# Performance work log

Measured on AMD Instinct MI355X. Metric: run time of the kernel, lower is better.

The kernel has to match this reference:

```python
import jax, jax.numpy as jnp
import numpy as np

N, E, C_IN, C_OUT = 50000, 800000, 64, 64
BN_EPS = 1e-5


def _batchnorm(h, gamma, beta):
    # Training-mode BatchNorm1d: batch statistics over dim 0, biased variance.
    mean = h.mean(axis=0)
    var = h.var(axis=0)  # ddof=0, matches PyTorch normalization stats
    return gamma * (h - mean) * jax.lax.rsqrt(var + BN_EPS) + beta


def setup_inputs() -> dict:
    key = jax.random.key(0)
    ks = jax.random.split(key, 6)
    x = jax.random.normal(ks[0], (N, C_IN), dtype=jnp.float32)
    edge_index = jax.random.randint(ks[1], (2, E), 0, N, dtype=jnp.int32)
    edge_weight = jax.random.uniform(ks[2], (E,), dtype=jnp.float32)
    s1 = 1.0 / np.sqrt(C_IN).astype(np.float32)
    s2 = 1.0 / np.sqrt(2 * C_IN).astype(np.float32)
    pool_W = jax.random.uniform(ks[3], (C_IN, C_IN), jnp.float32, -s1, s1)
    pool_b = jnp.zeros((C_IN,), jnp.float32)
    final_W = jax.random.uniform(ks[4], (2 * C_IN, C_OUT), jnp.float32, -s2, s2)
    final_b = jnp.zeros((C_OUT,), jnp.float32)
    return {
        "x": x,
        "edge_index": edge_index,
        "edge_weight": edge_weight,
        "pool_W": pool_W,
        "pool_b": pool_b,
        "bn_pool_gamma": jnp.ones((C_IN,), jnp.float32),
        "bn_pool_beta": jnp.zeros((C_IN,), jnp.float32),
        "final_W": final_W,
        "final_b": final_b,
        "bn_final_gamma": jnp.ones((C_OUT,), jnp.float32),
        "bn_final_beta": jnp.zeros((C_OUT,), jnp.float32),
        "coef": jnp.float32(0.5),
    }


def reference(x, edge_index, edge_weight, pool_W, pool_b, bn_pool_gamma,
              bn_pool_beta, final_W, final_b, bn_final_gamma, bn_final_beta,
              coef):
    src, dst = edge_index[0], edge_index[1]
    # gather src node features, scale by edge weight  -> [E, C_IN]
    edge_feat = x[src] * (1.0 + coef * edge_weight[:, None])
    pooled = edge_feat @ pool_W + pool_b              # [E, C_IN]
    pooled = jax.nn.relu(_batchnorm(pooled, bn_pool_gamma, bn_pool_beta))
    # scatter-max into destination nodes; empty segments -> 0 (pooled >= 0)
    agg = jax.ops.segment_max(pooled, dst, num_segments=x.shape[0])
    agg = jnp.maximum(agg, 0.0)                       # fill -inf (empty) with 0
    h = jnp.concatenate([x, agg], axis=-1) @ final_W + final_b  # [N, C_OUT]
    h = _batchnorm(h, bn_final_gamma, bn_final_beta)
    return jax.nn.relu(h)
```

## Files before the change

### kernel.cpp

```cpp
#include <hip/hip_runtime.h>
#include <hip/hip_fp16.h>
#include <math.h>
#include <float.h>

#define BN_EPS 1e-5f
#define SLOTS 64


typedef __attribute__((ext_vector_type(8))) short bf16x8;
typedef __attribute__((ext_vector_type(4))) float f32x4;

__device__ inline unsigned short f2bf(float f) {
    unsigned u = __float_as_uint(f);
    return (unsigned short)((u + 0x7fffu + ((u >> 16) & 1u)) >> 16);
}
__device__ inline float bf2f(unsigned short h) {
    return __uint_as_float(((unsigned)h) << 16);
}

__global__ __launch_bounds__(256) void k_scatter(const int* __restrict__ src,
                          const int* __restrict__ dst,
                          const float* __restrict__ w, const float* __restrict__ coef_p,
                          int* __restrict__ cnt, unsigned* __restrict__ csr, int E) {
    int i = blockIdx.x * blockDim.x + threadIdx.x;
    if (i >= E) return;
    const float coef = *coef_p;
    int sn = src[i], tn = dst[i];
    float s = fmaf(coef, w[i], 1.0f);
    unsigned hs = (unsigned)__half_as_ushort(__float2half(s));
    int pos = atomicAdd(&cnt[tn], 1);
    if (pos < SLOTS) csr[(size_t)tn * SLOTS + pos] = ((unsigned)sn << 16) | hs;
}

__global__ __launch_bounds__(256, 4) void k_gemm_pool(const float* __restrict__ x,
                            const float* __restrict__ W,
                            unsigned short* __restrict__ ybf, int nrows) {
    __shared__ unsigned short Wt[64 * 72];
    for (int i = threadIdx.x; i < 64 * 64; i += 256) {
        int k = i >> 6, n = i & 63;
        Wt[n * 72 + k] = f2bf(W[i]);
    }
    __syncthreads();
    const int lane = threadIdx.x & 63;
    const int wave = threadIdx.x >> 6;
    const int quad = lane >> 4;
    const int ln = lane & 15;
    bf16x8 Bf[2][4];
#pragma unroll
    for (int kc = 0; kc < 2; ++kc)
#pragma unroll
        for (int ct = 0; ct < 4; ++ct)
            Bf[kc][ct] = *(const bf16x8*)&Wt[(ct * 16 + ln) * 72 + kc * 32 + quad * 8];
    const int T = (nrows + 15) >> 4;
    const int gw = blockIdx.x * 4 + wave;
    const int nw = gridDim.x * 4;
    for (int t = gw; t < T; t += nw) {
        const int row = t * 16 + ln;
        bf16x8 af[2];
        if (row < nrows) {
            const float* xr = x + (size_t)row * 64;
#pragma unroll
            for (int kc = 0; kc < 2; ++kc) {
                float4 p = *(const float4*)(xr + kc * 32 + quad * 8);
                float4 q = *(const float4*)(xr + kc * 32 + quad * 8 + 4);
                bf16x8 a;
                a[0] = (short)f2bf(p.x); a[1] = (short)f2bf(p.y);
                a[2] = (short)f2bf(p.z); a[3] = (short)f2bf(p.w);
                a[4] = (short)f2bf(q.x); a[5] = (short)f2bf(q.y);
                a[6] = (short)f2bf(q.z); a[7] = (short)f2bf(q.w);
                af[kc] = a;
            }
        } else {
            bf16x8 z;
#pragma unroll
            for (int j = 0; j < 8; ++j) z[j] = 0;
            af[0] = z; af[1] = z;
        }
        f32x4 acc[4];
#pragma unroll
        for (int ct = 0; ct < 4; ++ct) { acc[ct][0]=0.f; acc[ct][1]=0.f; acc[ct][2]=0.f; acc[ct][3]=0.f; }
#pragma unroll
        for (int ct = 0; ct < 4; ++ct) {
            acc[ct] = __builtin_amdgcn_mfma_f32_16x16x32_bf16(af[0], Bf[0][ct], acc[ct], 0, 0, 0);
            acc[ct] = __builtin_amdgcn_mfma_f32_16x16x32_bf16(af[1], Bf[1][ct], acc[ct], 0, 0, 0);
        }
#pragma unroll
        for (int r = 0; r < 4; ++r) {
            int ro = t * 16 + quad * 4 + r;
            if (ro < nrows) {
#pragma unroll
                for (int ct = 0; ct < 4; ++ct)
                    ybf[(size_t)ro * 64 + ct * 16 + ln] = f2bf(acc[ct][r]);
            }
        }
    }
}

__global__ __launch_bounds__(256) void k_gather_max(const unsigned short* __restrict__ ybf,
                             const unsigned* __restrict__ csr, const int* __restrict__ cnt,
                             float* __restrict__ M, float* __restrict__ partials, int nrows) {
    int t = blockIdx.x * blockDim.x + threadIdx.x;
    int node = t >> 4;
    int sub = threadIdx.x & 15;
    int rg = threadIdx.x >> 4;
    int c0 = sub * 4;
    size_t base = (size_t)node * SLOTS;
    int dg = 0;
    if (node < nrows) { dg = cnt[node]; if (dg > SLOTS) dg = SLOTS; }
    float m0 = -FLT_MAX, m1 = -FLT_MAX, m2 = -FLT_MAX, m3 = -FLT_MAX;
    float s1[4] = {0, 0, 0, 0}, s2[4] = {0, 0, 0, 0};
    for (int k0 = 0; k0 < dg; k0 += 16) {
        int kk = k0 + sub;
        unsigned pk = (kk < dg) ? csr[base + kk] : 0u;
        int cnt16 = dg - k0; if (cnt16 > 16) cnt16 = 16;
        for (int j = 0; j < cnt16; ++j) {
            unsigned r = (unsigned)__shfl((int)pk, j, 16);
            int sn = r >> 16;
            float sv = __half2float(__ushort_as_half((unsigned short)(r & 0xffffu)));
            ushort4 uv = *(const ushort4*)&ybf[(size_t)sn * 64 + c0];
            float v0 = sv * bf2f(uv.x), v1 = sv * bf2f(uv.y);
            float v2 = sv * bf2f(uv.z), v3 = sv * bf2f(uv.w);
            m0 = fmaxf(m0, v0); s1[0] += v0; s2[0] = fmaf(v0, v0, s2[0]);
            m1 = fmaxf(m1, v1); s1[1] += v1; s2[1] = fmaf(v1, v1, s2[1]);
            m2 = fmaxf(m2, v2); s1[2] += v2; s2[2] = fmaf(v2, v2, s2[2]);
            m3 = fmaxf(m3, v3); s1[3] += v3; s2[3] = fmaf(v3, v3, s2[3]);
        }
    }
    if (node < nrows)
        *(float4*)&M[(size_t)node * 64 + c0] = make_float4(m0, m1, m2, m3);
    __shared__ float red[16][68];
#pragma unroll
    for (int j = 0; j < 4; ++j) red[rg][c0 + j] = s1[j];
    __syncthreads();
    if (rg == 0) {
#pragma unroll
        for (int j = 0; j < 4; ++j) {
            float tt = 0.0f;
            for (int r = 0; r < 16; ++r) tt += red[r][c0 + j];
            partials[(size_t)blockIdx.x * 128 + c0 + j] = tt;
        }
    }
    __syncthreads();
#pragma unroll
    for (int j = 0; j < 4; ++j) red[rg][c0 + j] = s2[j];
    __syncthreads();
    if (rg == 0) {
#pragma unroll
        for (int j = 0; j < 4; ++j) {
            float tt = 0.0f;
            for (int r = 0; r < 16; ++r) tt += red[r][c0 + j];
            partials[(size_t)blockIdx.x * 128 + 64 + c0 + j] = tt;
        }
    }
}

__global__ __launch_bounds__(256) void k_red1(const float* __restrict__ partials, int P,
                                              float* __restrict__ p2) {
    int c = threadIdx.x & 127;
    int half = threadIdx.x >> 7;
    float acc = 0.0f;
    for (int r = blockIdx.x * 2 + half; r < P; r += 256)
        acc += partials[(size_t)r * 128 + c];
    __shared__ float sh[256];
    sh[threadIdx.x] = acc;
    __syncthreads();
    if (half == 0) p2[(size_t)blockIdx.x * 128 + c] = sh[c] + sh[128 + c];
}

__global__ __launch_bounds__(1024) void k_red2(const float* __restrict__ p2,
                             const float* __restrict__ pool_b, const float* __restrict__ gamma,
                             const float* __restrict__ beta, float invE,
                             float* __restrict__ coef) {
    int c = threadIdx.x & 127;
    int seg = threadIdx.x >> 7;
    float acc = 0.0f;
    for (int r = seg; r < 128; r += 8) acc += p2[(size_t)r * 128 + c];
    __shared__ float red[8][128];
    red[seg][c] = acc;
    __syncthreads();
    if (seg == 0) {
        float tt = 0.0f;
#pragma unroll
        for (int s = 0; s < 8; ++s) tt += red[s][c];
        red[0][c] = tt;
    }
    __syncthreads();
    if (threadIdx.x < 64) {
        int c0 = threadIdx.x;
        float S1 = red[0][c0], S2 = red[0][64 + c0];
        float s1 = S1 * invE;
        float b = pool_b[c0];
        float mean = s1 + b;
        float ex2 = S2 * invE + 2.0f * b * s1 + b * b;
        float var = ex2 - mean * mean;
        float a = gamma[c0] * rsqrtf(var + BN_EPS);
        coef[c0] = a;
        coef[64 + c0] = beta[c0] - a * s1;
    }
}

__global__ __launch_bounds__(1024) void k_red2f(const float* __restrict__ p2,
                             const float* __restrict__ gamma, const float* __restrict__ beta,
                             float invN, float* __restrict__ coef) {
    int c = threadIdx.x & 127;
    int seg = threadIdx.x >> 7;
    float acc = 0.0f;
    for (int r = seg; r < 128; r += 8) acc += p2[(size_t)r * 128 + c];
    __shared__ float red[8][128];
    red[seg][c] = acc;
    __syncthreads();
    if (seg == 0) {
        float tt = 0.0f;
#pragma unroll
        for (int s = 0; s < 8; ++s) tt += red[s][c];
        red[0][c] = tt;
    }
    __syncthreads();
    if (threadIdx.x < 64) {
        int c0 = threadIdx.x;
        float mean = red[0][c0] * invN;
        float var = red[0][64 + c0] * invN - mean * mean;
        float a = gamma[c0] * rsqrtf(var + BN_EPS);
        coef[c0] = a;
        coef[64 + c0] = beta[c0] - a * mean;
    }
}

__global__ __launch_bounds__(256, 2) void k_final_gemm(const float* __restrict__ x,
                             const float* __restrict__ M, const float* __restrict__ coef,
                             const float* __restrict__ W, const float* __restrict__ b,
                             float* __restrict__ h, float* __restrict__ partials, int nrows) {
    __shared__ unsigned short Wt[64 * 136];
    __shared__ float hp[128];
    for (int i = threadIdx.x; i < 128 * 64; i += 256) {
        int k = i >> 6, n = i & 63;
        Wt[n * 136 + k] = f2bf(W[i]);
    }
    if (threadIdx.x < 128) hp[threadIdx.x] = 0.0f;
    __syncthreads();
    const int lane = threadIdx.x & 63;
    const int wave = threadIdx.x >> 6;
    const int quad = lane >> 4;
    const int ln = lane & 15;
    bf16x8 Bf[4][4];
#pragma unroll
    for (int kc = 0; kc < 4; ++kc)
#pragma unroll
        for (int ct = 0; ct < 4; ++ct)
            Bf[kc][ct] = *(const bf16x8*)&Wt[(ct * 16 + ln) * 136 + kc * 32 + quad * 8];
    float bias[4];
#pragma unroll
    for (int ct = 0; ct < 4; ++ct) bias[ct] = b[ct * 16 + ln];
    float ca[2][8], cd[2][8];
#pragma unroll
    for (int g = 0; g < 2; ++g) {
        int ch = g * 32 + quad * 8;
#pragma unroll
        for (int j = 0; j < 8; ++j) {
            ca[g][j] = coef[ch + j];
            cd[g][j] = coef[64 + ch + j];
        }
    }
    float ls1[4] = {0, 0, 0, 0}, ls2[4] = {0, 0, 0, 0};
    const int T = (nrows + 15) >> 4;
    const int gw = blockIdx.x * 4 + wave;
    const int nw = gridDim.x * 4;
    for (int t = gw; t < T; t += nw) {
        const int row = t * 16 + ln;
        bf16x8 af[4];
        if (row < nrows) {
            const float* xr = x + (size_t)row * 64;
#pragma unroll
            for (int kc = 0; kc < 2; ++kc) {
                float4 p = *(const float4*)(xr + kc * 32 + quad * 8);
                float4 q = *(const float4*)(xr + kc * 32 + quad * 8 + 4);
                bf16x8 a;
                a[0] = (short)f2bf(p.x); a[1] = (short)f2bf(p.y);
                a[2] = (short)f2bf(p.z); a[3] = (short)f2bf(p.w);
                a[4] = (short)f2bf(q.x); a[5] = (short)f2bf(q.y);
                a[6] = (short)f2bf(q.z); a[7] = (short)f2bf(q.w);
                af[kc] = a;
            }
            const float* mr = M + (size_t)row * 64;
#pragma unroll
            for (int g = 0; g < 2; ++g) {
                const float* mp = mr + g * 32 + quad * 8;
                float4 p = *(const float4*)mp;
                float4 q = *(const float4*)(mp + 4);
                float v[8] = {p.x, p.y, p.z, p.w, q.x, q.y, q.z, q.w};
                bf16x8 a;
#pragma unroll
                for (int j = 0; j < 8; ++j)
                    a[j] = (short)f2bf(fmaxf(fmaf(ca[g][j], v[j], cd[g][j]), 0.0f));
                af[2 + g] = a;
            }
        } else {
            bf16x8 z;
#pragma unroll
            for (int j = 0; j < 8; ++j) z[j] = 0;
#pragma unroll
            for (int kc = 0; kc < 4; ++kc) af[kc] = z;
        }
        f32x4 acc[4];
#pragma unroll
        for (int ct = 0; ct < 4; ++ct) { acc[ct][0]=0.f; acc[ct][1]=0.f; acc[ct][2]=0.f; acc[ct][3]=0.f; }
#pragma unroll
        for (int kc = 0; kc < 4; ++kc)
#pragma unroll
            for (int ct = 0; ct < 4; ++ct)
                acc[ct] = __builtin_amdgcn_mfma_f32_16x16x32_bf16(af[kc], Bf[kc][ct], acc[ct], 0, 0, 0);
#pragma unroll
        for (int r = 0; r < 4; ++r) {
            int ro = t * 16 + quad * 4 + r;
            if (ro < nrows) {
#pragma unroll
                for (int ct = 0; ct < 4; ++ct) {
                    float hv = acc[ct][r] + bias[ct];
                    h[(size_t)ro * 64 + ct * 16 + ln] = hv;
                    ls1[ct] += hv;
                    ls2[ct] = fmaf(hv, hv, ls2[ct]);
                }
            }
        }
    }
#pragma unroll
    for (int ct = 0; ct < 4; ++ct) {
        atomicAdd(&hp[ct * 16 + ln], ls1[ct]);
        atomicAdd(&hp[64 + ct * 16 + ln], ls2[ct]);
    }
    __syncthreads();
    if (threadIdx.x < 128)
        partials[(size_t)blockIdx.x * 128 + threadIdx.x] = hp[threadIdx.x];
}

__global__ __launch_bounds__(256) void k_bn_out(const float* __restrict__ h,
                         const float* __restrict__ coef,
                         float* __restrict__ out, int nrows) {
    const int idx = blockIdx.x * blockDim.x + threadIdx.x;
    const int total = nrows * 16;
    if (idx >= total) return;
    const int c0 = (idx & 15) * 4;
    const float4 hv = *(const float4*)(h + (size_t)idx * 4);
    float4 o;
    float* op = (float*)&o;
    const float* hp = (const float*)&hv;
#pragma unroll
    for (int j = 0; j < 4; ++j) {
        const int c = c0 + j;
        op[j] = fmaxf(fmaf(coef[c], hp[j], coef[64 + c]), 0.0f);
    }
    *(float4*)(out + (size_t)idx * 4) = o;
}

extern "C" void kernel_launch(void* const* d_in, const int* in_sizes, int n_in,
                              void* d_out, int out_size, void* d_ws, size_t ws_size,
                              hipStream_t stream) {
    const float* x       = (const float*)d_in[0];
    const int*   eidx    = (const int*)d_in[1];
    const float* ew      = (const float*)d_in[2];
    const float* pool_W  = (const float*)d_in[3];
    const float* pool_b  = (const float*)d_in[4];
    const float* g1      = (const float*)d_in[5];
    const float* b1      = (const float*)d_in[6];
    const float* final_W = (const float*)d_in[7];
    const float* final_b = (const float*)d_in[8];
    const float* g2      = (const float*)d_in[9];
    const float* b2      = (const float*)d_in[10];
    const float* coef    = (const float*)d_in[11];

    const int N = in_sizes[0] / 64;
    const int E = in_sizes[1] / 2;
    const int* src = eidx;
    const int* dst = eidx + E;

    const int PG  = (N * 16 + 255) / 256;
    const int T   = (N + 15) / 16;
    const int nbT = (T + 3) / 4;

    unsigned* ws = (unsigned*)d_ws;
    int*   cnt      = (int*)ws;
    float* bncoef   = (float*)(ws + (size_t)N);
    float* coef2    = (float*)(ws + (size_t)N + 128);
    float* p2       = (float*)(ws + (size_t)N + 256);
    float* p2F      = p2 + 16384;
    float* partialsG= p2F + 16384;
    float* partialsF= partialsG + (size_t)PG * 128;
    unsigned short* ybf = (unsigned short*)(partialsF + (size_t)nbT * 128);
    unsigned* csrF  = (unsigned*)ybf + (size_t)32 * N;
    float* M        = (float*)(csrF + (size_t)SLOTS * N);

    hipMemsetAsync(cnt, 0, (size_t)N * 4, stream);

    const int nb256 = (E + 255) / 256;

    k_scatter<<<nb256, 256, 0, stream>>>(src, dst, ew, coef, cnt, csrF, E);
    k_gemm_pool<<<nbT, 256, 0, stream>>>(x, pool_W, ybf, N);
    k_gather_max<<<PG, 256, 0, stream>>>(ybf, csrF, cnt, M, partialsG, N);
    k_red1   <<<128, 256, 0, stream>>>(partialsG, PG, p2);
    k_red2   <<<1, 1024, 0, stream>>>(p2, pool_b, g1, b1, 1.0f / (float)E, bncoef);
    k_final_gemm<<<nbT, 256, 0, stream>>>(x, M, bncoef, final_W, final_b,
                                          (float*)d_out, partialsF, N);
    k_red1   <<<128, 256, 0, stream>>>(partialsF, nbT, p2F);
    k_red2f  <<<1, 1024, 0, stream>>>(p2F, g2, b2, 1.0f / (float)N, coef2);
    k_bn_out <<<(N * 16 + 255) / 256, 256, 0, stream>>>((const float*)d_out, coef2,
                                                        (float*)d_out, N);
}
```

Measured before the change: 207.5 us.

## Fuse scatter and pool GEMM into one launch with dst-partitioned scatter blocks

Combines the CSR-bucketing scatter and the pool GEMM into a single kernel whose first SB blocks do the scatter and whose remaining blocks do the GEMM, so the two independent stages run concurrently. Scatter blocks are split into 8 groups by destination-node range, each group scanning all edges and handling only its own range, which localises the atomics and CSR writes. Each group re-reads the dst array in full, so dst traffic grows eightfold. The gather-max kernel becomes grid-stride over a fixed 1024 blocks, which also shrinks the partials reduction.

```diff
diff --git a/kernel.cpp b/kernel.cpp
--- a/kernel.cpp
+++ b/kernel.cpp
@@ -18,24 +18,34 @@
     return __uint_as_float(((unsigned)h) << 16);
 }
 
-__global__ __launch_bounds__(256) void k_scatter(const int* __restrict__ src,
-                          const int* __restrict__ dst,
-                          const float* __restrict__ w, const float* __restrict__ coef_p,
-                          int* __restrict__ cnt, unsigned* __restrict__ csr, int E) {
-    int i = blockIdx.x * blockDim.x + threadIdx.x;
-    if (i >= E) return;
-    const float coef = *coef_p;
-    int sn = src[i], tn = dst[i];
-    float s = fmaf(coef, w[i], 1.0f);
-    unsigned hs = (unsigned)__half_as_ushort(__float2half(s));
-    int pos = atomicAdd(&cnt[tn], 1);
-    if (pos < SLOTS) csr[(size_t)tn * SLOTS + pos] = ((unsigned)sn << 16) | hs;
-}
-
-__global__ __launch_bounds__(256, 4) void k_gemm_pool(const float* __restrict__ x,
-                            const float* __restrict__ W,
-                            unsigned short* __restrict__ ybf, int nrows) {
+__global__ __launch_bounds__(256, 4) void k_scatter_pool(
+        const int* __restrict__ src, const int* __restrict__ dst,
+        const float* __restrict__ w, const float* __restrict__ coef_p,
+        int* __restrict__ cnt, unsigned* __restrict__ csr, int E,
+        const float* __restrict__ x, const float* __restrict__ W,
+        unsigned short* __restrict__ ybf, int nrows, int SB) {
     __shared__ unsigned short Wt[64 * 72];
+    if ((int)blockIdx.x < SB) {
+        const int p = blockIdx.x & 7;
+        const int q = blockIdx.x >> 3;
+        const int SBq = SB >> 3;
+        const int Npart = (nrows + 7) >> 3;
+        const int lo = p * Npart;
+        const int hi = (lo + Npart < nrows) ? lo + Npart : nrows;
+        const float coef = *coef_p;
+        for (int i = q * 256 + threadIdx.x; i < E; i += SBq * 256) {
+            int tn = dst[i];
+            if (tn >= lo && tn < hi) {
+                int sn = src[i];
+                float s = fmaf(coef, w[i], 1.0f);
+                unsigned hs = (unsigned)__half_as_ushort(__float2half(s));
+                int pos = atomicAdd(&cnt[tn], 1);
+                if (pos < SLOTS)
+                    csr[(size_t)tn * SLOTS + pos] = ((unsigned)sn << 16) | hs;
+            }
+        }
+        return;
+    }
     for (int i = threadIdx.x; i < 64 * 64; i += 256) {
         int k = i >> 6, n = i & 63;
         Wt[n * 72 + k] = f2bf(W[i]);
@@ -52,8 +62,8 @@
         for (int ct = 0; ct < 4; ++ct)
             Bf[kc][ct] = *(const bf16x8*)&Wt[(ct * 16 + ln) * 72 + kc * 32 + quad * 8];
     const int T = (nrows + 15) >> 4;
-    const int gw = blockIdx.x * 4 + wave;
-    const int nw = gridDim.x * 4;
+    const int gw = ((int)blockIdx.x - SB) * 4 + wave;
+    const int nw = ((int)gridDim.x - SB) * 4;
     for (int t = gw; t < T; t += nw) {
         const int row = t * 16 + ln;
         bf16x8 af[2];
@@ -61,13 +71,13 @@
             const float* xr = x + (size_t)row * 64;
 #pragma unroll
             for (int kc = 0; kc < 2; ++kc) {
-                float4 p = *(const float4*)(xr + kc * 32 + quad * 8);
-                float4 q = *(const float4*)(xr + kc * 32 + quad * 8 + 4);
+                float4 pv = *(const float4*)(xr + kc * 32 + quad * 8);
+                float4 qv = *(const float4*)(xr + kc * 32 + quad * 8 + 4);
                 bf16x8 a;
-                a[0] = (short)f2bf(p.x); a[1] = (short)f2bf(p.y);
-                a[2] = (short)f2bf(p.z); a[3] = (short)f2bf(p.w);
-                a[4] = (short)f2bf(q.x); a[5] = (short)f2bf(q.y);
-                a[6] = (short)f2bf(q.z); a[7] = (short)f2bf(q.w);
+                a[0] = (short)f2bf(pv.x); a[1] = (short)f2bf(pv.y);
+                a[2] = (short)f2bf(pv.z); a[3] = (short)f2bf(pv.w);
+                a[4] = (short)f2bf(qv.x); a[5] = (short)f2bf(qv.y);
+                a[6] = (short)f2bf(qv.z); a[7] = (short)f2bf(qv.w);
                 af[kc] = a;
             }
         } else {
@@ -99,35 +109,37 @@
 __global__ __launch_bounds__(256) void k_gather_max(const unsigned short* __restrict__ ybf,
                              const unsigned* __restrict__ csr, const int* __restrict__ cnt,
                              float* __restrict__ M, float* __restrict__ partials, int nrows) {
-    int t = blockIdx.x * blockDim.x + threadIdx.x;
-    int node = t >> 4;
     int sub = threadIdx.x & 15;
     int rg = threadIdx.x >> 4;
     int c0 = sub * 4;
-    size_t base = (size_t)node * SLOTS;
-    int dg = 0;
-    if (node < nrows) { dg = cnt[node]; if (dg > SLOTS) dg = SLOTS; }
-    float m0 = -FLT_MAX, m1 = -FLT_MAX, m2 = -FLT_MAX, m3 = -FLT_MAX;
     float s1[4] = {0, 0, 0, 0}, s2[4] = {0, 0, 0, 0};
-    for (int k0 = 0; k0 < dg; k0 += 16) {
-        int kk = k0 + sub;
-        unsigned pk = (kk < dg) ? csr[base + kk] : 0u;
-        int cnt16 = dg - k0; if (cnt16 > 16) cnt16 = 16;
-        for (int j = 0; j < cnt16; ++j) {
-            unsigned r = (unsigned)__shfl((int)pk, j, 16);
-            int sn = r >> 16;
-            float sv = __half2float(__ushort_as_half((unsigned short)(r & 0xffffu)));
-            ushort4 uv = *(const ushort4*)&ybf[(size_t)sn * 64 + c0];
-            float v0 = sv * bf2f(uv.x), v1 = sv * bf2f(uv.y);
-            float v2 = sv * bf2f(uv.z), v3 = sv * bf2f(uv.w);
-            m0 = fmaxf(m0, v0); s1[0] += v0; s2[0] = fmaf(v0, v0, s2[0]);
-            m1 = fmaxf(m1, v1); s1[1] += v1; s2[1] = fmaf(v1, v1, s2[1]);
-            m2 = fmaxf(m2, v2); s1[2] += v2; s2[2] = fmaf(v2, v2, s2[2]);
-            m3 = fmaxf(m3, v3); s1[3] += v3; s2[3] = fmaf(v3, v3, s2[3]);
-        }
-    }
-    if (node < nrows)
-        *(float4*)&M[(size_t)node * 64 + c0] = make_float4(m0, m1, m2, m3);
+    const int nchunks = (nrows + 15) >> 4;
+    for (int nb = blockIdx.x; nb < nchunks; nb += gridDim.x) {
+        int node = nb * 16 + rg;
+        size_t base = (size_t)node * SLOTS;
+        int dg = 0;
+        if (node < nrows) { dg = cnt[node]; if (dg > SLOTS) dg = SLOTS; }
+        float m0 = -FLT_MAX, m1 = -FLT_MAX, m2 = -FLT_MAX, m3 = -FLT_MAX;
+        for (int k0 = 0; k0 < dg; k0 += 16) {
+            int kk = k0 + sub;
+            unsigned pk = (kk < dg) ? csr[base + kk] : 0u;
+            int cnt16 = dg - k0; if (cnt16 > 16) cnt16 = 16;
+            for (int j = 0; j < cnt16; ++j) {
+                unsigned r = (unsigned)__shfl((int)pk, j, 16);
+                int sn = r >> 16;
+                float sv = __half2float(__ushort_as_half((unsigned short)(r & 0xffffu)));
+                ushort4 uv = *(const ushort4*)&ybf[(size_t)sn * 64 + c0];
+                float v0 = sv * bf2f(uv.x), v1 = sv * bf2f(uv.y);
+                float v2 = sv * bf2f(uv.z), v3 = sv * bf2f(uv.w);
+                m0 = fmaxf(m0, v0); s1[0] += v0; s2[0] = fmaf(v0, v0, s2[0]);
+                m1 = fmaxf(m1, v1); s1[1] += v1; s2[1] = fmaf(v1, v1, s2[1]);
+                m2 = fmaxf(m2, v2); s1[2] += v2; s2[2] = fmaf(v2, v2, s2[2]);
+                m3 = fmaxf(m3, v3); s1[3] += v3; s2[3] = fmaf(v3, v3, s2[3]);
+            }
+        }
+        if (node < nrows)
+            *(float4*)&M[(size_t)node * 64 + c0] = make_float4(m0, m1, m2, m3);
+    }
     __shared__ float red[16][68];
 #pragma unroll
     for (int j = 0; j < 4; ++j) red[rg][c0 + j] = s1[j];
@@ -272,22 +284,22 @@
             const float* xr = x + (size_t)row * 64;
 #pragma unroll
             for (int kc = 0; kc < 2; ++kc) {
-                float4 p = *(const float4*)(xr + kc * 32 + quad * 8);
-                float4 q = *(const float4*)(xr + kc * 32 + quad * 8 + 4);
+                float4 pv = *(const float4*)(xr + kc * 32 + quad * 8);
+                float4 qv = *(const float4*)(xr + kc * 32 + quad * 8 + 4);
                 bf16x8 a;
-                a[0] = (short)f2bf(p.x); a[1] = (short)f2bf(p.y);
-                a[2] = (short)f2bf(p.z); a[3] = (short)f2bf(p.w);
-                a[4] = (short)f2bf(q.x); a[5] = (short)f2bf(q.y);
-                a[6] = (short)f2bf(q.z); a[7] = (short)f2bf(q.w);
+                a[0] = (short)f2bf(pv.x); a[1] = (short)f2bf(pv.y);
+                a[2] = (short)f2bf(pv.z); a[3] = (short)f2bf(pv.w);
+                a[4] = (short)f2bf(qv.x); a[5] = (short)f2bf(qv.y);
+                a[6] = (short)f2bf(qv.z); a[7] = (short)f2bf(qv.w);
                 af[kc] = a;
             }
             const float* mr = M + (size_t)row * 64;
 #pragma unroll
             for (int g = 0; g < 2; ++g) {
                 const float* mp = mr + g * 32 + quad * 8;
-                float4 p = *(const float4*)mp;
-                float4 q = *(const float4*)(mp + 4);
-                float v[8] = {p.x, p.y, p.z, p.w, q.x, q.y, q.z, q.w};
+                float4 pv = *(const float4*)mp;
+                float4 qv = *(const float4*)(mp + 4);
+                float v[8] = {pv.x, pv.y, pv.z, pv.w, qv.x, qv.y, qv.z, qv.w};
                 bf16x8 a;
 #pragma unroll
                 for (int j = 0; j < 8; ++j)
@@ -373,9 +385,10 @@
     const int* src = eidx;
     const int* dst = eidx + E;
 
-    const int PG  = (N * 16 + 255) / 256;
+    const int SB  = 2048;
     const int T   = (N + 15) / 16;
     const int nbT = (T + 3) / 4;
+    const int PG  = 1024;
 
     unsigned* ws = (unsigned*)d_ws;
     int*   cnt      = (int*)ws;
@@ -391,10 +404,8 @@
 
     hipMemsetAsync(cnt, 0, (size_t)N * 4, stream);
 
-    const int nb256 = (E + 255) / 256;
-
-    k_scatter<<<nb256, 256, 0, stream>>>(src, dst, ew, coef, cnt, csrF, E);
-    k_gemm_pool<<<nbT, 256, 0, stream>>>(x, pool_W, ybf, N);
+    k_scatter_pool<<<SB + nbT, 256, 0, stream>>>(src, dst, ew, coef, cnt, csrF, E,
+                                                 x, pool_W, ybf, N, SB);
     k_gather_max<<<PG, 256, 0, stream>>>(ybf, csrF, cnt, M, partialsG, N);
     k_red1   <<<128, 256, 0, stream>>>(partialsG, PG, p2);
     k_red2   <<<1, 1024, 0, stream>>>(p2, pool_b, g1, b1, 1.0f / (float)E, bncoef);
```

New measurement: 218.7 us. +5.4%, slower.
